# Optimization experiments

Measured on AMD Instinct MI355X. Metric: run time of the kernel, lower is better.

The kernel has to match this reference:

```python
import jax, jax.numpy as jnp
import numpy as np

B, T = 512, 16385  # batch, num_samples; fitted window M = T - 1


def setup_inputs() -> dict:
    key = jax.random.key(0)
    k1, _ = jax.random.split(key)
    # positive samples so ny + cumsum(x) stays > 0 (needed for u**r and log u)
    x = jax.random.uniform(k1, (B, 1, T), dtype=jnp.float32)
    params = jnp.array([0.5, 1.0], dtype=jnp.float32)  # [r, ny]
    return {"x": x, "params": params}


def _cusum(x, h):
    # trapezoidal cumulative integral: y[0]=0, y[t]=y[t-1]+0.5*h*(x[t-1]+x[t])
    inc = 0.5 * h * (x[..., :-1] + x[..., 1:])
    zero = jnp.zeros(x.shape[:-1] + (1,), x.dtype)
    return jnp.concatenate([zero, jnp.cumsum(inc, axis=-1)], axis=-1)


def reference(x, params):
    r, ny = params[0], params[1]
    y = _cusum(x, 1.0)              # (B, 1, T)
    u = ny + y[:, 0, 1:]            # (B, M) ; M = T-1
    phi = jnp.stack([u, u ** r], axis=1)   # (B, 2, M) basis
    phip = jnp.linalg.pinv(phi)            # (B, M, 2)
    xd = x[:, :, 1:]                        # (B, 1, M)
    coeffs = xd @ phip                      # (B, 1, 2)
    x_hat = coeffs @ phi                    # (B, 1, M)
    res = xd - x_hat                        # (B, 1, M)
    r2 = jnp.sum(res ** 2, axis=-1)         # (B, 1)
    return coeffs, x_hat, res, r2
```

## Files before the change

kernel.cpp:

```cpp
#include <hip/hip_runtime.h>
#include <hip/hip_bf16.h>

#define TPB 512
#define VPT 32
#define NDAT 16384
#define TLEN 16385
#define NW (TPB / 64)

__global__ __launch_bounds__(TPB) void vpl_kernel(
    const float* __restrict__ x, const float* __restrict__ params,
    float* __restrict__ out, int B) {
  const int b = blockIdx.x;
  const int tid = threadIdx.x;
  const int lane = tid & 63;
  const int wid = tid >> 6;

  const float r = params[0];
  const float ny = params[1];
  const bool rhalf = (r == 0.5f);

  const float* __restrict__ xr = x + (size_t)b * TLEN;

  float* out_coeffs = out;
  float* out_xhat = out + (size_t)2 * B + (size_t)b * NDAT;
  float* out_res = out + (size_t)2 * B + (size_t)B * NDAT + (size_t)b * NDAT;
  float* out_r2 = out + (size_t)2 * B + (size_t)2 * B * NDAT;

  __shared__ double wtot[NW];
  __shared__ double sred[NW][5];
  __shared__ float cbc[2];

  const int base = tid * VPT;

  const float x0 = xr[base];
  float xv[VPT];
#pragma unroll
  for (int j = 0; j < VPT; ++j) xv[j] = xr[base + 1 + j];

  float run[VPT];
  {
    float prev = x0, acc = 0.f;
#pragma unroll
    for (int j = 0; j < VPT; ++j) {
      acc += 0.5f * (prev + xv[j]);
      run[j] = acc;
      prev = xv[j];
    }
  }
  const float tot = run[VPT - 1];

  double t = (double)tot;
#pragma unroll
  for (int d = 1; d < 64; d <<= 1) {
    double o = __shfl_up(t, d, 64);
    if (lane >= d) t += o;
  }
  if (lane == 63) wtot[wid] = t;
  __syncthreads();

  double cross = 0.0;
#pragma unroll
  for (int w = 0; w < NW; ++w)
    if (w < wid) cross += wtot[w];
  const float offf = (float)((double)ny + cross + (t - (double)tot));

  float s_u = 0.f, s_u2 = 0.f, s_u15 = 0.f, s_xu = 0.f, s_xv = 0.f;
  if (rhalf) {
#pragma unroll
    for (int j = 0; j < VPT; ++j) {
      const float uu = offf + run[j];
      const float vh = sqrtf(uu);
      const float xd = xv[j];
      s_u += uu;
      s_u2 = fmaf(uu, uu, s_u2);
      s_u15 = fmaf(uu, vh, s_u15);
      s_xu = fmaf(xd, uu, s_xu);
      s_xv = fmaf(xd, vh, s_xv);
    }
  } else {
#pragma unroll
    for (int j = 0; j < VPT; ++j) {
      const float uu = offf + run[j];
      const float vh = powf(uu, r);
      const float xd = xv[j];
      s_u += uu;
      s_u2 = fmaf(uu, uu, s_u2);
      s_u15 = fmaf(uu, vh, s_u15);
      s_xu = fmaf(xd, uu, s_xu);
      s_xv = fmaf(xd, vh, s_xv);
    }
  }

  {
    double vals[5] = {(double)s_u, (double)s_u2, (double)s_u15, (double)s_xu,
                      (double)s_xv};
#pragma unroll
    for (int i = 0; i < 5; ++i) {
      double v = vals[i];
#pragma unroll
      for (int d = 32; d >= 1; d >>= 1) v += __shfl_down(v, d, 64);
      vals[i] = v;
    }
    if (lane == 0) {
#pragma unroll
      for (int i = 0; i < 5; ++i) sred[wid][i] = vals[i];
    }
  }
  __syncthreads();

  if (tid == 0) {
    double g[5];
#pragma unroll
    for (int i = 0; i < 5; ++i) {
      double s = 0.0;
#pragma unroll
      for (int w = 0; w < NW; ++w) s += sred[w][i];
      g[i] = s;
    }
    const double g11 = g[0];
    const double g00 = g[1];
    const double g01 = g[2];
    const double b0 = g[3];
    const double b1 = g[4];

    const double tr = g00 + g11;
    const double det = g00 * g11 - g01 * g01;
    const double disc = sqrt(fmax(tr * tr - 4.0 * det, 0.0));
    const double l1 = 0.5 * (tr + disc);
    const double l2 = (l1 > 0.0) ? fmax(det / l1, 0.0) : 0.0;
    const double s1 = sqrt(fmax(l1, 0.0));
    const double s2 = sqrt(l2);
    const double rcond = 0.01953125;

    double c0, c1;
    if (s2 > rcond * s1) {
      c0 = (g11 * b0 - g01 * b1) / det;
      c1 = (g00 * b1 - g01 * b0) / det;
    } else if (s1 > 0.0) {
      double w0 = l1 - g11, w1 = g01;
      double nrm = sqrt(w0 * w0 + w1 * w1);
      double e0, e1;
      if (nrm > 0.0) {
        e0 = w0 / nrm;
        e1 = w1 / nrm;
      } else {
        e0 = 1.0;
        e1 = 0.0;
      }
      const double gam = (b0 * e0 + b1 * e1) / l1;
      c0 = gam * e0;
      c1 = gam * e1;
    } else {
      c0 = 0.0;
      c1 = 0.0;
    }
    out_coeffs[2 * b] = (float)c0;
    out_coeffs[2 * b + 1] = (float)c1;
    cbc[0] = (float)c0;
    cbc[1] = (float)c1;
  }
  __syncthreads();
  const float c0 = cbc[0];
  const float c1 = cbc[1];

  float r2f = 0.f;
  if (rhalf) {
#pragma unroll
    for (int q = 0; q < VPT / 4; ++q) {
      float xh[4], rs[4];
#pragma unroll
      for (int i = 0; i < 4; ++i) {
        const int j = q * 4 + i;
        const float uu = offf + run[j];
        const float vh = sqrtf(uu);
        xh[i] = fmaf(c0, uu, c1 * vh);
        rs[i] = xv[j] - xh[i];
        r2f = fmaf(rs[i], rs[i], r2f);
      }
      *reinterpret_cast<float4*>(out_xhat + base + 4 * q) =
          make_float4(xh[0], xh[1], xh[2], xh[3]);
      *reinterpret_cast<float4*>(out_res + base + 4 * q) =
          make_float4(rs[0], rs[1], rs[2], rs[3]);
    }
  } else {
#pragma unroll
    for (int q = 0; q < VPT / 4; ++q) {
      float xh[4], rs[4];
#pragma unroll
      for (int i = 0; i < 4; ++i) {
        const int j = q * 4 + i;
        const float uu = offf + run[j];
        const float vh = powf(uu, r);
        xh[i] = fmaf(c0, uu, c1 * vh);
        rs[i] = xv[j] - xh[i];
        r2f = fmaf(rs[i], rs[i], r2f);
      }
      *reinterpret_cast<float4*>(out_xhat + base + 4 * q) =
          make_float4(xh[0], xh[1], xh[2], xh[3]);
      *reinterpret_cast<float4*>(out_res + base + 4 * q) =
          make_float4(rs[0], rs[1], rs[2], rs[3]);
    }
  }

  double r2 = (double)r2f;
#pragma unroll
  for (int d = 32; d >= 1; d >>= 1) r2 += __shfl_down(r2, d, 64);
  if (lane == 0) sred[wid][0] = r2;
  __syncthreads();
  if (tid == 0) {
    double s = 0.0;
#pragma unroll
    for (int w = 0; w < NW; ++w) s += sred[w][0];
    out_r2[b] = (float)s;
  }
}

extern "C" void kernel_launch(void* const* d_in, const int* in_sizes, int n_in,
                              void* d_out, int out_size, void* d_ws,
                              size_t ws_size, hipStream_t stream) {
  const float* x = (const float*)d_in[0];
  const float* params = (const float*)d_in[1];
  float* out = (float*)d_out;
  const int B = in_sizes[0] / TLEN;
  vpl_kernel<<<dim3(B), dim3(TPB), 0, stream>>>(x, params, out, B);
}
```

Baseline: 119.8 us.

## Split each row across four blocks using a three-kernel scan/gram/output pipeline

Replaces the single one-block-per-row kernel with three kernels. Each row is split into four chunks handled by separate 256-thread blocks: chunk totals first, then per-chunk Gram partial sums using the cross-chunk offsets, then coefficients, outputs and r2 accumulated with atomics. The aim is more parallelism and less register pressure per thread. In exchange, x is read three times, there are two extra launches, and r2 summation order changes through float atomics.

```diff
diff --git a/kernel.cpp b/kernel.cpp
--- a/kernel.cpp
+++ b/kernel.cpp
@@ -1,76 +1,99 @@
 #include <hip/hip_runtime.h>
-#include <hip/hip_bf16.h>
-
-#define TPB 512
-#define VPT 32
+
 #define NDAT 16384
 #define TLEN 16385
+#define CPR 4
+#define CHUNK (NDAT / CPR)
+#define TPB 256
+#define VPT (CHUNK / TPB)
 #define NW (TPB / 64)
 
-__global__ __launch_bounds__(TPB) void vpl_kernel(
-    const float* __restrict__ x, const float* __restrict__ params,
-    float* __restrict__ out, int B) {
-  const int b = blockIdx.x;
-  const int tid = threadIdx.x;
-  const int lane = tid & 63;
-  const int wid = tid >> 6;
-
-  const float r = params[0];
-  const float ny = params[1];
+__device__ __forceinline__ double wave_sum_f64(double v) {
+#pragma unroll
+  for (int d = 32; d >= 1; d >>= 1) v += __shfl_down(v, d, 64);
+  return v;
+}
+
+__global__ __launch_bounds__(TPB) void k_tot(const float* __restrict__ x,
+                                             double* __restrict__ wsTot,
+                                             float* __restrict__ out_r2,
+                                             int B) {
+  const int blk = blockIdx.x;
+  const int row = blk / CPR, c = blk % CPR;
+  const int tid = threadIdx.x, lane = tid & 63, wid = tid >> 6;
+  const float* __restrict__ xr = x + (size_t)row * TLEN + c * CHUNK;
+  const int base = tid * VPT;
+
+  float xs[VPT + 1];
+#pragma unroll
+  for (int j = 0; j <= VPT; ++j) xs[j] = xr[base + j];
+  float acc = 0.f;
+#pragma unroll
+  for (int j = 0; j < VPT; ++j) acc += 0.5f * (xs[j] + xs[j + 1]);
+
+  __shared__ double swav[NW];
+  const double t = wave_sum_f64((double)acc);
+  if (lane == 0) swav[wid] = t;
+  if (blk == 0) {
+    for (int i = tid; i < B; i += TPB) out_r2[i] = 0.f;
+  }
+  __syncthreads();
+  if (tid == 0) {
+    double s = 0.0;
+#pragma unroll
+    for (int w = 0; w < NW; ++w) s += swav[w];
+    wsTot[blk] = s;
+  }
+}
+
+__global__ __launch_bounds__(TPB) void k_gram(const float* __restrict__ x,
+                                              const float* __restrict__ params,
+                                              const double* __restrict__ wsTot,
+                                              double* __restrict__ wsGram) {
+  const int blk = blockIdx.x;
+  const int row = blk / CPR, c = blk % CPR;
+  const int tid = threadIdx.x, lane = tid & 63, wid = tid >> 6;
+  const float r = params[0], ny = params[1];
   const bool rhalf = (r == 0.5f);
-
-  const float* __restrict__ xr = x + (size_t)b * TLEN;
-
-  float* out_coeffs = out;
-  float* out_xhat = out + (size_t)2 * B + (size_t)b * NDAT;
-  float* out_res = out + (size_t)2 * B + (size_t)B * NDAT + (size_t)b * NDAT;
-  float* out_r2 = out + (size_t)2 * B + (size_t)2 * B * NDAT;
-
-  __shared__ double wtot[NW];
-  __shared__ double sred[NW][5];
-  __shared__ float cbc[2];
-
+  const float* __restrict__ xr = x + (size_t)row * TLEN + c * CHUNK;
   const int base = tid * VPT;
 
-  const float x0 = xr[base];
-  float xv[VPT];
-#pragma unroll
-  for (int j = 0; j < VPT; ++j) xv[j] = xr[base + 1 + j];
-
-  float run[VPT];
-  {
-    float prev = x0, acc = 0.f;
-#pragma unroll
-    for (int j = 0; j < VPT; ++j) {
-      acc += 0.5f * (prev + xv[j]);
-      run[j] = acc;
-      prev = xv[j];
-    }
-  }
-  const float tot = run[VPT - 1];
-
-  double t = (double)tot;
+  float xs[VPT + 1];
+#pragma unroll
+  for (int j = 0; j <= VPT; ++j) xs[j] = xr[base + j];
+  float tf = 0.f;
+#pragma unroll
+  for (int j = 0; j < VPT; ++j) tf += 0.5f * (xs[j] + xs[j + 1]);
+
+  double t = (double)tf;
 #pragma unroll
   for (int d = 1; d < 64; d <<= 1) {
     double o = __shfl_up(t, d, 64);
     if (lane >= d) t += o;
   }
-  if (lane == 63) wtot[wid] = t;
-  __syncthreads();
-
+  __shared__ double swav[NW];
+  if (lane == 63) swav[wid] = t;
+  __syncthreads();
+
+  double cOff = (double)ny;
+#pragma unroll
+  for (int cc = 0; cc < CPR; ++cc)
+    if (cc < c) cOff += wsTot[row * CPR + cc];
   double cross = 0.0;
 #pragma unroll
   for (int w = 0; w < NW; ++w)
-    if (w < wid) cross += wtot[w];
-  const float offf = (float)((double)ny + cross + (t - (double)tot));
+    if (w < wid) cross += swav[w];
+  const float offf = (float)(cOff + cross + (t - (double)tf));
 
   float s_u = 0.f, s_u2 = 0.f, s_u15 = 0.f, s_xu = 0.f, s_xv = 0.f;
   if (rhalf) {
+    float acc = 0.f;
 #pragma unroll
     for (int j = 0; j < VPT; ++j) {
-      const float uu = offf + run[j];
+      acc += 0.5f * (xs[j] + xs[j + 1]);
+      const float uu = offf + acc;
       const float vh = sqrtf(uu);
-      const float xd = xv[j];
+      const float xd = xs[j + 1];
       s_u += uu;
       s_u2 = fmaf(uu, uu, s_u2);
       s_u15 = fmaf(uu, vh, s_u15);
@@ -78,11 +101,13 @@
       s_xv = fmaf(xd, vh, s_xv);
     }
   } else {
+    float acc = 0.f;
 #pragma unroll
     for (int j = 0; j < VPT; ++j) {
-      const float uu = offf + run[j];
+      acc += 0.5f * (xs[j] + xs[j + 1]);
+      const float uu = offf + acc;
       const float vh = powf(uu, r);
-      const float xd = xv[j];
+      const float xd = xs[j + 1];
       s_u += uu;
       s_u2 = fmaf(uu, uu, s_u2);
       s_u15 = fmaf(uu, vh, s_u15);
@@ -91,31 +116,74 @@
     }
   }
 
-  {
-    double vals[5] = {(double)s_u, (double)s_u2, (double)s_u15, (double)s_xu,
-                      (double)s_xv};
-#pragma unroll
-    for (int i = 0; i < 5; ++i) {
-      double v = vals[i];
-#pragma unroll
-      for (int d = 32; d >= 1; d >>= 1) v += __shfl_down(v, d, 64);
-      vals[i] = v;
-    }
-    if (lane == 0) {
-#pragma unroll
-      for (int i = 0; i < 5; ++i) sred[wid][i] = vals[i];
-    }
-  }
-  __syncthreads();
-
+  __shared__ double sred[NW][5];
+  double vals[5] = {(double)s_u, (double)s_u2, (double)s_u15, (double)s_xu,
+                    (double)s_xv};
+#pragma unroll
+  for (int i = 0; i < 5; ++i) vals[i] = wave_sum_f64(vals[i]);
+  if (lane == 0) {
+#pragma unroll
+    for (int i = 0; i < 5; ++i) sred[wid][i] = vals[i];
+  }
+  __syncthreads();
   if (tid == 0) {
-    double g[5];
 #pragma unroll
     for (int i = 0; i < 5; ++i) {
       double s = 0.0;
 #pragma unroll
       for (int w = 0; w < NW; ++w) s += sred[w][i];
-      g[i] = s;
+      wsGram[(size_t)blk * 5 + i] = s;
+    }
+  }
+}
+
+__global__ __launch_bounds__(TPB) void k_out(
+    const float* __restrict__ x, const float* __restrict__ params,
+    const double* __restrict__ wsTot, const double* __restrict__ wsGram,
+    float* __restrict__ out_coeffs, float* __restrict__ out_xhat,
+    float* __restrict__ out_res, float* __restrict__ out_r2) {
+  const int blk = blockIdx.x;
+  const int row = blk / CPR, c = blk % CPR;
+  const int tid = threadIdx.x, lane = tid & 63, wid = tid >> 6;
+  const float r = params[0], ny = params[1];
+  const bool rhalf = (r == 0.5f);
+  const float* __restrict__ xr = x + (size_t)row * TLEN + c * CHUNK;
+  const int base = tid * VPT;
+
+  float xs[VPT + 1];
+#pragma unroll
+  for (int j = 0; j <= VPT; ++j) xs[j] = xr[base + j];
+  float tf = 0.f;
+#pragma unroll
+  for (int j = 0; j < VPT; ++j) tf += 0.5f * (xs[j] + xs[j + 1]);
+
+  double t = (double)tf;
+#pragma unroll
+  for (int d = 1; d < 64; d <<= 1) {
+    double o = __shfl_up(t, d, 64);
+    if (lane >= d) t += o;
+  }
+  __shared__ double swav[NW];
+  __shared__ float cbc[2];
+  if (lane == 63) swav[wid] = t;
+  __syncthreads();
+
+  double cOff = (double)ny;
+#pragma unroll
+  for (int cc = 0; cc < CPR; ++cc)
+    if (cc < c) cOff += wsTot[row * CPR + cc];
+  double cross = 0.0;
+#pragma unroll
+  for (int w = 0; w < NW; ++w)
+    if (w < wid) cross += swav[w];
+  const float offf = (float)(cOff + cross + (t - (double)tf));
+
+  if (tid == 0) {
+    double g[5] = {0.0, 0.0, 0.0, 0.0, 0.0};
+    for (int cc = 0; cc < CPR; ++cc) {
+#pragma unroll
+      for (int i = 0; i < 5; ++i)
+        g[i] += wsGram[((size_t)row * CPR + cc) * 5 + i];
     }
     const double g11 = g[0];
     const double g00 = g[1];
@@ -139,13 +207,10 @@
     } else if (s1 > 0.0) {
       double w0 = l1 - g11, w1 = g01;
       double nrm = sqrt(w0 * w0 + w1 * w1);
-      double e0, e1;
+      double e0 = 1.0, e1 = 0.0;
       if (nrm > 0.0) {
         e0 = w0 / nrm;
         e1 = w1 / nrm;
-      } else {
-        e0 = 1.0;
-        e1 = 0.0;
       }
       const double gam = (b0 * e0 + b1 * e1) / l1;
       c0 = gam * e0;
@@ -154,64 +219,72 @@
       c0 = 0.0;
       c1 = 0.0;
     }
-    out_coeffs[2 * b] = (float)c0;
-    out_coeffs[2 * b + 1] = (float)c1;
     cbc[0] = (float)c0;
     cbc[1] = (float)c1;
+    if (c == 0) {
+      out_coeffs[2 * row] = (float)c0;
+      out_coeffs[2 * row + 1] = (float)c1;
+    }
   }
   __syncthreads();
   const float c0 = cbc[0];
   const float c1 = cbc[1];
 
+  float* __restrict__ oxh = out_xhat + (size_t)row * NDAT + c * CHUNK + base;
+  float* __restrict__ ors = out_res + (size_t)row * NDAT + c * CHUNK + base;
+
   float r2f = 0.f;
   if (rhalf) {
+    float acc = 0.f;
 #pragma unroll
     for (int q = 0; q < VPT / 4; ++q) {
       float xh[4], rs[4];
 #pragma unroll
       for (int i = 0; i < 4; ++i) {
         const int j = q * 4 + i;
-        const float uu = offf + run[j];
+        acc += 0.5f * (xs[j] + xs[j + 1]);
+        const float uu = offf + acc;
         const float vh = sqrtf(uu);
         xh[i] = fmaf(c0, uu, c1 * vh);
-        rs[i] = xv[j] - xh[i];
+        rs[i] = xs[j + 1] - xh[i];
         r2f = fmaf(rs[i], rs[i], r2f);
       }
-      *reinterpret_cast<float4*>(out_xhat + base + 4 * q) =
+      *reinterpret_cast<float4*>(oxh + 4 * q) =
           make_float4(xh[0], xh[1], xh[2], xh[3]);
-      *reinterpret_cast<float4*>(out_res + base + 4 * q) =
+      *reinterpret_cast<float4*>(ors + 4 * q) =
           make_float4(rs[0], rs[1], rs[2], rs[3]);
     }
   } else {
+    float acc = 0.f;
 #pragma unroll
     for (int q = 0; q < VPT / 4; ++q) {
       float xh[4], rs[4];
 #pragma unroll
       for (int i = 0; i < 4; ++i) {
         const int j = q * 4 + i;
-        const float uu = offf + run[j];
+        acc += 0.5f * (xs[j] + xs[j + 1]);
+        const float uu = offf + acc;
         const float vh = powf(uu, r);
         xh[i] = fmaf(c0, uu, c1 * vh);
-        rs[i] = xv[j] - xh[i];
+        rs[i] = xs[j + 1] - xh[i];
         r2f = fmaf(rs[i], rs[i], r2f);
       }
-      *reinterpret_cast<float4*>(out_xhat + base + 4 * q) =
+      *reinterpret_cast<float4*>(oxh + 4 * q) =
           make_float4(xh[0], xh[1], xh[2], xh[3]);
-      *reinterpret_cast<float4*>(out_res + base + 4 * q) =
+      *reinterpret_cast<float4*>(ors + 4 * q) =
           make_float4(rs[0], rs[1], rs[2], rs[3]);
     }
   }
 
-  double r2 = (double)r2f;
-#pragma unroll
-  for (int d = 32; d >= 1; d >>= 1) r2 += __shfl_down(r2, d, 64);
-  if (lane == 0) sred[wid][0] = r2;
+  __shared__ double sr2[NW];
+  const double r2 = wave_sum_f64((double)r2f);
+  if (lane == 0) sr2[wid] = r2;
   __syncthreads();
   if (tid == 0) {
     double s = 0.0;
 #pragma unroll
-    for (int w = 0; w < NW; ++w) s += sred[w][0];
-    out_r2[b] = (float)s;
+    for (int w = 0; w < NW; ++w) s += sr2[w];
+    atomicAdd(out_r2 + row, (float)s);
   }
 }
 
@@ -222,5 +295,19 @@
   const float* params = (const float*)d_in[1];
   float* out = (float*)d_out;
   const int B = in_sizes[0] / TLEN;
-  vpl_kernel<<<dim3(B), dim3(TPB), 0, stream>>>(x, params, out, B);
-}
+  const int nblk = B * CPR;
+
+  float* out_coeffs = out;
+  float* out_xhat = out + (size_t)2 * B;
+  float* out_res = out + (size_t)2 * B + (size_t)B * NDAT;
+  float* out_r2 = out + (size_t)2 * B + (size_t)2 * B * NDAT;
+
+  double* wsTot = (double*)d_ws;
+  double* wsGram = (double*)d_ws + nblk;
+
+  k_tot<<<dim3(nblk), dim3(TPB), 0, stream>>>(x, wsTot, out_r2, B);
+  k_gram<<<dim3(nblk), dim3(TPB), 0, stream>>>(x, params, wsTot, wsGram);
+  k_out<<<dim3(nblk), dim3(TPB), 0, stream>>>(x, params, wsTot, wsGram,
+                                              out_coeffs, out_xhat, out_res,
+                                              out_r2);
+}
```

Measured after the change: 120.7 us. Within noise of the previous version (+0.7%).
